# Performance work log

Measured on AMD Instinct MI355X. Metric: run time of the kernel, lower is better.

## Reference

```python
import jax, jax.numpy as jnp
import numpy as np

H = 2048          # hidden_size
M = 512           # moe_intermediate_size
E = 8             # n_routed_experts
TOP_K = 2         # num_experts_per_tok
N_SHARED = 2      # n_shared_experts -> shared intermediate = M * N_SHARED
MS = M * N_SHARED
B, S = 2, 1024


def setup_inputs() -> dict:
    key = jax.random.key(0)
    ks = jax.random.split(key, 9)
    sc = 0.02
    return {
        "hidden_states": jax.random.normal(ks[0], (B, S, H), dtype=jnp.float32),
        "gate_w": jax.random.normal(ks[1], (E, H), dtype=jnp.float32) * sc,
        "Wg": jax.random.normal(ks[2], (E, H, M), dtype=jnp.float32) * sc,   # gate_proj per expert
        "Wu": jax.random.normal(ks[3], (E, H, M), dtype=jnp.float32) * sc,   # up_proj per expert
        "Wd": jax.random.normal(ks[4], (E, M, H), dtype=jnp.float32) * sc,   # down_proj per expert
        "sWg": jax.random.normal(ks[5], (H, MS), dtype=jnp.float32) * sc,    # shared gate_proj
        "sWu": jax.random.normal(ks[6], (H, MS), dtype=jnp.float32) * sc,    # shared up_proj
        "sWd": jax.random.normal(ks[7], (MS, H), dtype=jnp.float32) * sc,    # shared down_proj
    }


def reference(hidden_states, gate_w, Wg, Wu, Wd, sWg, sWu, sWd):
    b, s, h = hidden_states.shape
    x = hidden_states.reshape(-1, h)                     # [N, H]
    n = x.shape[0]

    # --- MoEGate: top-k routing with softmax over the selected logits ---
    logits = x @ gate_w.T                                # [N, E]
    topk_vals, topk_idx = jax.lax.top_k(logits, TOP_K)   # [N, K]
    w = jax.nn.softmax(topk_vals, axis=-1)               # softmax scoring over top-k
    # per-token combine weight for every expert (zero where not routed)
    comb = jnp.zeros((n, E), x.dtype).at[jnp.arange(n)[:, None], topk_idx].add(w)

    # --- Routed experts (SwiGLU MLP per expert); combine is the sparse
    #     weight matrix `comb`, mathematically identical to torch dispatch ---
    g = jnp.einsum('nh,ehm->enm', x, Wg)                 # [E, N, M]
    u = jnp.einsum('nh,ehm->enm', x, Wu)
    eo = jnp.einsum('enm,emh->enh', jax.nn.silu(g) * u, Wd)  # [E, N, H]
    y = jnp.einsum('ne,enh->nh', comb, eo)               # weighted combine

    # --- Shared experts (dense SwiGLU MLP on all tokens) ---
    y = y + (jax.nn.silu(x @ sWg) * (x @ sWu)) @ sWd
    return y.reshape(b, s, h)
```

## Files before the change

kernel.cpp:

```cpp
#include <hip/hip_runtime.h>

#define H 2048
#define MDIM 512
#define NE 8
#define MS 1024
#define NTOK 2048
#define ACT_R_ROWS 5120

typedef unsigned short u16;
typedef __attribute__((ext_vector_type(8))) short s16x8;
typedef __attribute__((ext_vector_type(4))) float f32x4;

__device__ inline u16 f2bf(float f) {
  unsigned u = __builtin_bit_cast(unsigned, f);
  u = (u + 0x7fffu + ((u >> 16) & 1u)) >> 16;
  return (u16)u;
}
__device__ inline float bf2f(u16 v) {
  return __builtin_bit_cast(float, (unsigned)v << 16);
}

__device__ inline f32x4 mfma16(s16x8 a, s16x8 b, f32x4 c) {
  return __builtin_amdgcn_mfma_f32_16x16x32_bf16(a, b, c, 0, 0, 0);
}

__device__ inline void gload16(const void* g, void* l) {
  __builtin_amdgcn_global_load_lds(
      (const __attribute__((address_space(1))) unsigned int*)g,
      (__attribute__((address_space(3))) unsigned int*)l, 16, 0, 0);
}


__global__ void k_cvt(const float* __restrict__ src, u16* __restrict__ dst, int n8) {
  int i = blockIdx.x * 256 + threadIdx.x;
  if (i >= n8) return;
  const f32x4* s = (const f32x4*)src;
  f32x4 a = s[2 * i + 0], b = s[2 * i + 1];
  s16x8 o;
  o[0] = (short)f2bf(a[0]); o[1] = (short)f2bf(a[1]);
  o[2] = (short)f2bf(a[2]); o[3] = (short)f2bf(a[3]);
  o[4] = (short)f2bf(b[0]); o[5] = (short)f2bf(b[1]);
  o[6] = (short)f2bf(b[2]); o[7] = (short)f2bf(b[3]);
  ((s16x8*)dst)[i] = o;
}

__device__ inline void tile_t64(const float* __restrict__ src, u16* __restrict__ dst,
                                int R, int C, int bx, int by) {
  __shared__ u16 tt[64][66];
  int c0 = bx * 64, r0 = by * 64;
  int t = threadIdx.x;
  int cq = (t & 15) * 4, rr = t >> 4;
  #pragma unroll
  for (int i = 0; i < 4; i++) {
    int row = rr + i * 16;
    f32x4 v = *(const f32x4*)&src[(long)(r0 + row) * C + c0 + cq];
    tt[cq + 0][row] = f2bf(v[0]);
    tt[cq + 1][row] = f2bf(v[1]);
    tt[cq + 2][row] = f2bf(v[2]);
    tt[cq + 3][row] = f2bf(v[3]);
  }
  __syncthreads();
  int c = t >> 2, ch = t & 3;
  #pragma unroll
  for (int h = 0; h < 2; h++) {
    int chunk = ch + h * 4;
    const u16* p = &tt[c][chunk * 8];
    s16x8 o;
    #pragma unroll
    for (int w0 = 0; w0 < 8; w0++) o[w0] = (short)p[w0];
    *(s16x8*)&dst[(long)(c0 + c) * R + r0 + chunk * 8] = o;
  }
}

__global__ __launch_bounds__(256) void k_prep(
    const float* __restrict__ Wg, const float* __restrict__ Wu,
    const float* __restrict__ Wd, const float* __restrict__ sWg,
    const float* __restrict__ sWu, const float* __restrict__ sWd,
    u16* __restrict__ WgT, u16* __restrict__ WuT, u16* __restrict__ WdT,
    u16* __restrict__ sWgT, u16* __restrict__ sWuT, u16* __restrict__ sWdT) {
  int b = blockIdx.x;
  const float* src; u16* dst; int R, C, lb;
  if (b < 2048) {
    lb = b; R = H; C = MDIM;
    int z = lb >> 8; lb &= 255;
    src = Wg + (size_t)z * H * MDIM; dst = WgT + (size_t)z * MDIM * H;
  } else if (b < 4096) {
    lb = b - 2048; R = H; C = MDIM;
    int z = lb >> 8; lb &= 255;
    src = Wu + (size_t)z * H * MDIM; dst = WuT + (size_t)z * MDIM * H;
  } else if (b < 6144) {
    lb = b - 4096; R = MDIM; C = H;
    int z = lb >> 8; lb &= 255;
    src = Wd + (size_t)z * MDIM * H; dst = WdT + (size_t)z * H * MDIM;
  } else if (b < 6656) {
    lb = b - 6144; R = H; C = MS; src = sWg; dst = sWgT;
  } else if (b < 7168) {
    lb = b - 6656; R = H; C = MS; src = sWu; dst = sWuT;
  } else {
    lb = b - 7168; R = MS; C = H; src = sWd; dst = sWdT;
  }
  int nbx = C >> 6;
  tile_t64(src, dst, R, C, lb % nbx, lb / nbx);
}


__global__ void k_logits(const float* __restrict__ x, const float* __restrict__ gw,
                         int* __restrict__ te, float* __restrict__ tw) {
  int n = blockIdx.x * 4 + (threadIdx.x >> 6);
  int lane = threadIdx.x & 63;
  double acc[NE];
  #pragma unroll
  for (int e = 0; e < NE; e++) acc[e] = 0.0;
  for (int j = lane; j < H; j += 64) {
    float xv = x[(long)n * H + j];
    #pragma unroll
    for (int e = 0; e < NE; e++) acc[e] += (double)xv * (double)gw[e * H + j];
  }
  #pragma unroll
  for (int off = 32; off; off >>= 1) {
    #pragma unroll
    for (int e = 0; e < NE; e++) acc[e] += __shfl_xor(acc[e], off);
  }
  if (lane == 0) {
    int b0 = 0; double v0 = acc[0];
    #pragma unroll
    for (int e = 1; e < NE; e++) { if (acc[e] > v0) { v0 = acc[e]; b0 = e; } }
    int b1 = -1; double v1 = -1e300;
    #pragma unroll
    for (int e = 0; e < NE; e++) { if (e != b0 && acc[e] > v1) { v1 = acc[e]; b1 = e; } }
    double ex = exp(v1 - v0);
    te[n * 2] = b0; te[n * 2 + 1] = b1;
    tw[n * 2] = (float)(1.0 / (1.0 + ex));
    tw[n * 2 + 1] = (float)(ex / (1.0 + ex));
  }
}

__global__ __launch_bounds__(256) void k_build(
    const int* __restrict__ te, const float* __restrict__ tw,
    int* __restrict__ counts, int* __restrict__ offs,
    int* __restrict__ perm, float* __restrict__ wgt, int* __restrict__ slotmap) {
  __shared__ int cnt[256][NE];
  __shared__ int pb[NE];
  int t = threadIdx.x;
  int ebuf[16];
  int lc[NE];
  #pragma unroll
  for (int e = 0; e < NE; e++) lc[e] = 0;
  #pragma unroll
  for (int i = 0; i < 16; i++) {
    int ei = te[t * 16 + i];
    ebuf[i] = ei;
    #pragma unroll
    for (int e = 0; e < NE; e++) lc[e] += (ei == e) ? 1 : 0;
  }
  #pragma unroll
  for (int e = 0; e < NE; e++) cnt[t][e] = lc[e];
  __syncthreads();
  if (t < NE) {
    int run = 0;
    for (int i = 0; i < 256; i++) { int v = cnt[i][t]; cnt[i][t] = run; run += v; }
    counts[t] = run;
  }
  __syncthreads();
  if (t == 0) {
    int off = 0;
    #pragma unroll
    for (int e = 0; e < NE; e++) {
      pb[e] = off; offs[e] = off;
      off += ((counts[e] + 127) >> 7) << 7;
    }
    offs[NE] = off;
  }
  for (int i = t; i < ACT_R_ROWS; i += 256) { perm[i] = 0; wgt[i] = 0.f; }
  __syncthreads();
  int run2[NE];
  #pragma unroll
  for (int e = 0; e < NE; e++) run2[e] = cnt[t][e];
  #pragma unroll
  for (int i = 0; i < 16; i++) {
    int ei = ebuf[i];
    int idx = 0;
    #pragma unroll
    for (int e = 0; e < NE; e++) {
      if (ei == e) idx = pb[e] + run2[e];
      run2[e] += (ei == e) ? 1 : 0;
    }
    perm[idx] = (t * 16 + i) >> 1;
    wgt[idx] = tw[t * 16 + i];
    slotmap[t * 16 + i] = idx;
  }
}

__global__ __launch_bounds__(256, 2) void k_gu(
    const u16* __restrict__ xbf, const u16* __restrict__ WgT, const u16* __restrict__ WuT,
    const u16* __restrict__ sWgT, const u16* __restrict__ sWuT,
    u16* __restrict__ act_s, u16* __restrict__ act_r,
    const int* __restrict__ perm, const int* __restrict__ counts,
    const int* __restrict__ offs) {
  int lin = blockIdx.x;
  int xcd = lin & 7, jj = lin >> 3;
  int g = xcd + 8 * (jj % 10);
  int bx = jj / 10;
  const u16 *Bg, *Bu;
  u16* act;
  int Nout, cnt, rowBase, by;
  bool gather;
  if (g < 16) {
    gather = false; by = g;
    cnt = NTOK; rowBase = bx * 128;
    Bg = sWgT + (size_t)by * 64 * H;
    Bu = sWuT + (size_t)by * 64 * H;
    act = act_s; Nout = MS;
  } else {
    gather = true;
    int e = (g - 16) >> 3; by = (g - 16) & 7;
    cnt = counts[e];
    if (bx * 128 >= cnt) return;
    rowBase = offs[e] + bx * 128;
    Bg = WgT + ((size_t)e * MDIM + (size_t)by * 64) * H;
    Bu = WuT + ((size_t)e * MDIM + (size_t)by * 64) * H;
    act = act_r; Nout = MDIM;
  }

  __shared__ char lds[2][32768];

  int tid = threadIdx.x;
  int wave = tid >> 6, lane = tid & 63;
  int wr = wave >> 1, wc = wave & 1;
  int la = lane & 15, ks = lane >> 4;

  int rIn = tid >> 3;
  int csrc = ((tid & 7) << 4) ^ ((rIn & 7) << 4);
  const char* srcA[4];
  const char* srcBg[2];
  const char* srcBu[2];
  #pragma unroll
  for (int j = 0; j < 4; j++) {
    int row = j * 32 + rIn;
    int tok = gather ? perm[rowBase + row] : (rowBase + row);
    srcA[j] = (const char*)xbf + (size_t)tok * H * 2 + csrc;
  }
  #pragma unroll
  for (int j = 0; j < 2; j++) {
    int row = j * 32 + rIn;
    srcBg[j] = (const char*)Bg + (size_t)row * H * 2 + csrc;
    srcBu[j] = (const char*)Bu + (size_t)row * H * 2 + csrc;
  }

  int offA[4][2], offB[2][2];
  #pragma unroll
  for (int m = 0; m < 4; m++) {
    int arow = wr * 64 + m * 16 + la;
    #pragma unroll
    for (int kk = 0; kk < 2; kk++) {
      int c = kk * 64 + ks * 16;
      offA[m][kk] = arow * 128 + (c ^ ((arow & 7) << 4));
    }
  }
  #pragma unroll
  for (int n = 0; n < 2; n++) {
    int brow = wc * 32 + n * 16 + la;
    #pragma unroll
    for (int kk = 0; kk < 2; kk++) {
      int c = kk * 64 + ks * 16;
      offB[n][kk] = brow * 128 + (c ^ ((brow & 7) << 4));
    }
  }

  f32x4 zero4 = {0.f, 0.f, 0.f, 0.f};
  f32x4 gacc[4][2], uacc[4][2];
  #pragma unroll
  for (int m = 0; m < 4; m++)
    #pragma unroll
    for (int n = 0; n < 2; n++) { gacc[m][n] = zero4; uacc[m][n] = zero4; }

  auto STAGE = [&](int p, int k0) {
    char* b = lds[p];
    #pragma unroll
    for (int j = 0; j < 4; j++)
      gload16(srcA[j] + k0, b + j * 4096 + wave * 1024);
    #pragma unroll
    for (int j = 0; j < 2; j++) {
      gload16(srcBg[j] + k0, b + 16384 + j * 4096 + wave * 1024);
      gload16(srcBu[j] + k0, b + 24576 + j * 4096 + wave * 1024);
    }
  };

  const int NT = H / 64;
  STAGE(0, 0);
  STAGE(1, 128);
  asm volatile("s_waitcnt vmcnt(8)" ::: "memory");
  __builtin_amdgcn_sched_barrier(0);
  __builtin_amdgcn_s_barrier();

  for (int t = 0; t < NT; ++t) {
    int p = t & 1;
    const char* A = lds[p];
    const char* G = lds[p] + 16384;
    const char* U = lds[p] + 24576;
    s16x8 af[2][4], gf[2][2], uf[2][2];
    #pragma unroll
    for (int kk = 0; kk < 2; kk++) {
      #pragma unroll
      for (int m = 0; m < 4; m++) af[kk][m] = *(const s16x8*)(A + offA[m][kk]);
      #pragma unroll
      for (int n = 0; n < 2; n++) {
        gf[kk][n] = *(const s16x8*)(G + offB[n][kk]);
        uf[kk][n] = *(const s16x8*)(U + offB[n][kk]);
      }
    }
    asm volatile("s_waitcnt lgkmcnt(0)" ::: "memory");
    __builtin_amdgcn_sched_barrier(0);
    __builtin_amdgcn_s_barrier();
    if (t + 2 < NT) STAGE(p, (t + 2) * 128);
    __builtin_amdgcn_sched_barrier(0);
    #pragma unroll
    for (int kk = 0; kk < 2; kk++) {
      #pragma unroll
      for (int m = 0; m < 4; m++) {
        #pragma unroll
        for (int n = 0; n < 2; n++) {
          gacc[m][n] = mfma16(af[kk][m], gf[kk][n], gacc[m][n]);
          uacc[m][n] = mfma16(af[kk][m], uf[kk][n], uacc[m][n]);
        }
      }
    }
    if (t + 2 < NT) { asm volatile("s_waitcnt vmcnt(8)" ::: "memory"); }
    else            { asm volatile("s_waitcnt vmcnt(0)" ::: "memory"); }
    __builtin_amdgcn_sched_barrier(0);
    __builtin_amdgcn_s_barrier();
  }

  #pragma unroll
  for (int m = 0; m < 4; m++) {
    #pragma unroll
    for (int n = 0; n < 2; n++) {
      #pragma unroll
      for (int r = 0; r < 4; r++) {
        int lr = wr * 64 + m * 16 + ks * 4 + r;
        int col = by * 64 + wc * 32 + n * 16 + la;
        float gg = gacc[m][n][r], uu = uacc[m][n][r];
        float a = gg / (1.0f + __expf(-gg)) * uu;
        if (gather && (bx * 128 + lr) >= cnt) a = 0.0f;
        act[(size_t)(rowBase + lr) * Nout + col] = f2bf(a);
      }
    }
  }
}

__global__ __launch_bounds__(256, 3) void k_down2(
    const u16* __restrict__ act_s, const u16* __restrict__ act_r,
    const u16* __restrict__ sWdT, const u16* __restrict__ WdT,
    float* __restrict__ y, u16* __restrict__ rdown,
    const float* __restrict__ wgt,
    const int* __restrict__ counts, const int* __restrict__ offs) {
  int lin = blockIdx.x;
  int xcd = lin & 7, jj = lin >> 3;
  int g = xcd + 8 * (jj % 36);
  int bx = jj / 36;
  const u16 *A, *B;
  int KD, NT, cnt, rowBase, by;
  bool routed;
  if (g < 32) {
    routed = false; by = g;
    KD = MS; NT = MS / 64;
    cnt = NTOK; rowBase = bx * 128;
    A = act_s + (size_t)rowBase * MS;
    B = sWdT + (size_t)by * 64 * MS;
  } else {
    routed = true;
    int e = (g - 32) >> 5; by = (g - 32) & 31;
    KD = MDIM; NT = MDIM / 64;
    cnt = counts[e];
    if (bx * 128 >= cnt) return;
    rowBase = offs[e] + bx * 128;
    A = act_r + (size_t)rowBase * MDIM;
    B = WdT + ((size_t)e * H + (size_t)by * 64) * MDIM;
  }

  __shared__ char lds[2][24576];

  int tid = threadIdx.x;
  int wave = tid >> 6, lane = tid & 63;
  int wr = wave >> 1, wc = wave & 1;
  int la = lane & 15, ks = lane >> 4;

  int rIn = tid >> 3;
  int csrc = ((tid & 7) << 4) ^ ((rIn & 7) << 4);
  const char* srcA[4];
  const char* srcB[2];
  #pragma unroll
  for (int j = 0; j < 4; j++) {
    int row = j * 32 + rIn;
    srcA[j] = (const char*)A + (size_t)row * KD * 2 + csrc;
  }
  #pragma unroll
  for (int j = 0; j < 2; j++) {
    int row = j * 32 + rIn;
    srcB[j] = (const char*)B + (size_t)row * KD * 2 + csrc;
  }

  int offA[4][2], offB[2][2];
  #pragma unroll
  for (int m = 0; m < 4; m++) {
    int arow = wr * 64 + m * 16 + la;
    #pragma unroll
    for (int kk = 0; kk < 2; kk++) {
      int c = kk * 64 + ks * 16;
      offA[m][kk] = arow * 128 + (c ^ ((arow & 7) << 4));
    }
  }
  #pragma unroll
  for (int n = 0; n < 2; n++) {
    int brow = wc * 32 + n * 16 + la;
    #pragma unroll
    for (int kk = 0; kk < 2; kk++) {
      int c = kk * 64 + ks * 16;
      offB[n][kk] = brow * 128 + (c ^ ((brow & 7) << 4));
    }
  }

  f32x4 zero4 = {0.f, 0.f, 0.f, 0.f};
  f32x4 acc[4][2];
  #pragma unroll
  for (int m = 0; m < 4; m++)
    #pragma unroll
    for (int n = 0; n < 2; n++) acc[m][n] = zero4;

  auto STAGE = [&](int p, int k0) {
    char* b = lds[p];
    #pragma unroll
    for (int j = 0; j < 4; j++)
      gload16(srcA[j] + k0, b + j * 4096 + wave * 1024);
    #pragma unroll
    for (int j = 0; j < 2; j++)
      gload16(srcB[j] + k0, b + 16384 + j * 4096 + wave * 1024);
  };

  STAGE(0, 0);
  STAGE(1, 128);
  asm volatile("s_waitcnt vmcnt(6)" ::: "memory");
  __builtin_amdgcn_sched_barrier(0);
  __builtin_amdgcn_s_barrier();

  for (int t = 0; t < NT; ++t) {
    int p = t & 1;
    const char* Ab = lds[p];
    const char* Bb = lds[p] + 16384;
    s16x8 af[2][4], bf[2][2];
    #pragma unroll
    for (int kk = 0; kk < 2; kk++) {
      #pragma unroll
      for (int m = 0; m < 4; m++) af[kk][m] = *(const s16x8*)(Ab + offA[m][kk]);
      #pragma unroll
      for (int n = 0; n < 2; n++) bf[kk][n] = *(const s16x8*)(Bb + offB[n][kk]);
    }
    asm volatile("s_waitcnt lgkmcnt(0)" ::: "memory");
    __builtin_amdgcn_sched_barrier(0);
    __builtin_amdgcn_s_barrier();
    if (t + 2 < NT) STAGE(p, (t + 2) * 128);
    __builtin_amdgcn_sched_barrier(0);
    #pragma unroll
    for (int kk = 0; kk < 2; kk++) {
      #pragma unroll
      for (int m = 0; m < 4; m++)
        #pragma unroll
        for (int n = 0; n < 2; n++) acc[m][n] = mfma16(af[kk][m], bf[kk][n], acc[m][n]);
    }
    if (t + 2 < NT) { asm volatile("s_waitcnt vmcnt(6)" ::: "memory"); }
    else            { asm volatile("s_waitcnt vmcnt(0)" ::: "memory"); }
    __builtin_amdgcn_sched_barrier(0);
    __builtin_amdgcn_s_barrier();
  }

  #pragma unroll
  for (int m = 0; m < 4; m++) {
    #pragma unroll
    for (int n = 0; n < 2; n++) {
      #pragma unroll
      for (int r = 0; r < 4; r++) {
        int lr = wr * 64 + m * 16 + ks * 4 + r;
        int col = by * 64 + wc * 32 + n * 16 + la;
        float v = acc[m][n][r];
        if (routed) {
          if (bx * 128 + lr < cnt) {
            int si = rowBase + lr;
            rdown[(size_t)si * H + col] = f2bf(wgt[si] * v);
          }
        } else {
          y[(size_t)(rowBase + lr) * H + col] = v;
        }
      }
    }
  }
}

__global__ __launch_bounds__(256) void k_combine(float* __restrict__ y,
                                                 const u16* __restrict__ rdown,
                                                 const int* __restrict__ slotmap) {
  int n = blockIdx.x;
  int s0 = slotmap[n * 2], s1 = slotmap[n * 2 + 1];
  const s16x8* r0 = (const s16x8*)(rdown + (size_t)s0 * H);
  const s16x8* r1 = (const s16x8*)(rdown + (size_t)s1 * H);
  f32x4* yp = (f32x4*)(y + (size_t)n * H);
  int t = threadIdx.x;
  s16x8 a = r0[t], b = r1[t];
  f32x4 y0 = yp[2 * t], y1 = yp[2 * t + 1];
  #pragma unroll
  for (int j = 0; j < 4; j++) {
    y0[j] += bf2f((u16)a[j]) + bf2f((u16)b[j]);
    y1[j] += bf2f((u16)a[4 + j]) + bf2f((u16)b[4 + j]);
  }
  yp[2 * t] = y0;
  yp[2 * t + 1] = y1;
}


extern "C" void kernel_launch(void* const* d_in, const int* in_sizes, int n_in,
                              void* d_out, int out_size, void* d_ws, size_t ws_size,
                              hipStream_t stream) {
  const float* x   = (const float*)d_in[0];
  const float* gw  = (const float*)d_in[1];
  const float* Wg  = (const float*)d_in[2];
  const float* Wu  = (const float*)d_in[3];
  const float* Wd  = (const float*)d_in[4];
  const float* sWg = (const float*)d_in[5];
  const float* sWu = (const float*)d_in[6];
  const float* sWd = (const float*)d_in[7];
  float* y = (float*)d_out;

  char* w = (char*)d_ws;
  auto alloc = [&](size_t bytes) {
    char* p = w;
    w += (bytes + 255) & ~(size_t)255;
    return p;
  };
  u16* xbf   = (u16*)alloc((size_t)NTOK * H * 2);
  u16* WgT   = (u16*)alloc((size_t)NE * MDIM * H * 2);
  u16* WuT   = (u16*)alloc((size_t)NE * MDIM * H * 2);
  u16* WdT   = (u16*)alloc((size_t)NE * H * MDIM * 2);
  u16* sWgT  = (u16*)alloc((size_t)MS * H * 2);
  u16* sWuT  = (u16*)alloc((size_t)MS * H * 2);
  u16* sWdT  = (u16*)alloc((size_t)H * MS * 2);
  u16* act_s = (u16*)alloc((size_t)NTOK * MS * 2);
  u16* act_r = (u16*)alloc((size_t)ACT_R_ROWS * MDIM * 2);
  u16* rdown = (u16*)alloc((size_t)ACT_R_ROWS * H * 2);
  int*   te      = (int*)alloc((size_t)NTOK * 2 * 4);
  float* tw      = (float*)alloc((size_t)NTOK * 2 * 4);
  int*   counts  = (int*)alloc(64);
  int*   offs    = (int*)alloc(64);
  int*   perm    = (int*)alloc((size_t)ACT_R_ROWS * 4);
  float* wgt     = (float*)alloc((size_t)ACT_R_ROWS * 4);
  int*   slotmap = (int*)alloc((size_t)NTOK * 2 * 4);

  k_logits<<<NTOK / 4, 256, 0, stream>>>(x, gw, te, tw);
  k_build<<<1, 256, 0, stream>>>(te, tw, counts, offs, perm, wgt, slotmap);

  int n8 = NTOK * H / 8;
  k_cvt<<<(n8 + 255) / 256, 256, 0, stream>>>(x, xbf, n8);
  k_prep<<<7680, 256, 0, stream>>>(Wg, Wu, Wd, sWg, sWu, sWd,
                                   WgT, WuT, WdT, sWgT, sWuT, sWdT);

  k_gu<<<80 * 16, 256, 0, stream>>>(
      xbf, WgT, WuT, sWgT, sWuT, act_s, act_r, perm, counts, offs);

  k_down2<<<288 * 16, 256, 0, stream>>>(
      act_s, act_r, sWdT, WdT, y, rdown, wgt, counts, offs);

  k_combine<<<NTOK, 256, 0, stream>>>(y, rdown, slotmap);
}
```

Measured before the change: 168.6 us.

## Fuse x conversion into logits kernel; single-buffer GEMM LDS for higher occupancy

```diff
diff --git a/kernel.cpp b/kernel.cpp
--- a/kernel.cpp
+++ b/kernel.cpp
@@ -8,6 +8,7 @@
 #define ACT_R_ROWS 5120
 
 typedef unsigned short u16;
+typedef __attribute__((ext_vector_type(4))) short s16x4;
 typedef __attribute__((ext_vector_type(8))) short s16x8;
 typedef __attribute__((ext_vector_type(4))) float f32x4;
 
@@ -31,18 +32,107 @@
 }
 
 
-__global__ void k_cvt(const float* __restrict__ src, u16* __restrict__ dst, int n8) {
-  int i = blockIdx.x * 256 + threadIdx.x;
-  if (i >= n8) return;
-  const f32x4* s = (const f32x4*)src;
-  f32x4 a = s[2 * i + 0], b = s[2 * i + 1];
-  s16x8 o;
-  o[0] = (short)f2bf(a[0]); o[1] = (short)f2bf(a[1]);
-  o[2] = (short)f2bf(a[2]); o[3] = (short)f2bf(a[3]);
-  o[4] = (short)f2bf(b[0]); o[5] = (short)f2bf(b[1]);
-  o[6] = (short)f2bf(b[2]); o[7] = (short)f2bf(b[3]);
-  ((s16x8*)dst)[i] = o;
-}
+__global__ __launch_bounds__(256) void k_xlog(const float* __restrict__ x,
+                                              const float* __restrict__ gw,
+                                              u16* __restrict__ xbf,
+                                              int* __restrict__ te, float* __restrict__ tw) {
+  int n = blockIdx.x * 4 + (threadIdx.x >> 6);
+  int lane = threadIdx.x & 63;
+  double acc[NE];
+  #pragma unroll
+  for (int e = 0; e < NE; e++) acc[e] = 0.0;
+  const f32x4* xr = (const f32x4*)(x + (size_t)n * H);
+  s16x4* xo = (s16x4*)(xbf + (size_t)n * H);
+  #pragma unroll
+  for (int it = 0; it < H / 256; it++) {
+    int j4 = it * 64 + lane;
+    f32x4 v = xr[j4];
+    s16x4 o;
+    o[0] = (short)f2bf(v[0]); o[1] = (short)f2bf(v[1]);
+    o[2] = (short)f2bf(v[2]); o[3] = (short)f2bf(v[3]);
+    xo[j4] = o;
+    #pragma unroll
+    for (int e = 0; e < NE; e++) {
+      f32x4 g = *(const f32x4*)&gw[e * H + j4 * 4];
+      acc[e] += (double)v[0] * g[0] + (double)v[1] * g[1] +
+                (double)v[2] * g[2] + (double)v[3] * g[3];
+    }
+  }
+  #pragma unroll
+  for (int off = 32; off; off >>= 1) {
+    #pragma unroll
+    for (int e = 0; e < NE; e++) acc[e] += __shfl_xor(acc[e], off);
+  }
+  if (lane == 0) {
+    int b0 = 0; double v0 = acc[0];
+    #pragma unroll
+    for (int e = 1; e < NE; e++) { if (acc[e] > v0) { v0 = acc[e]; b0 = e; } }
+    int b1 = -1; double v1 = -1e300;
+    #pragma unroll
+    for (int e = 0; e < NE; e++) { if (e != b0 && acc[e] > v1) { v1 = acc[e]; b1 = e; } }
+    double ex = exp(v1 - v0);
+    te[n * 2] = b0; te[n * 2 + 1] = b1;
+    tw[n * 2] = (float)(1.0 / (1.0 + ex));
+    tw[n * 2 + 1] = (float)(ex / (1.0 + ex));
+  }
+}
+
+__global__ __launch_bounds__(256) void k_build(
+    const int* __restrict__ te, const float* __restrict__ tw,
+    int* __restrict__ counts, int* __restrict__ offs,
+    int* __restrict__ perm, float* __restrict__ wgt, int* __restrict__ slotmap) {
+  __shared__ int cnt[256][NE];
+  __shared__ int pb[NE];
+  int t = threadIdx.x;
+  int ebuf[16];
+  int lc[NE];
+  #pragma unroll
+  for (int e = 0; e < NE; e++) lc[e] = 0;
+  #pragma unroll
+  for (int i = 0; i < 16; i++) {
+    int ei = te[t * 16 + i];
+    ebuf[i] = ei;
+    #pragma unroll
+    for (int e = 0; e < NE; e++) lc[e] += (ei == e) ? 1 : 0;
+  }
+  #pragma unroll
+  for (int e = 0; e < NE; e++) cnt[t][e] = lc[e];
+  __syncthreads();
+  if (t < NE) {
+    int run = 0;
+    for (int i = 0; i < 256; i++) { int v = cnt[i][t]; cnt[i][t] = run; run += v; }
+    counts[t] = run;
+  }
+  __syncthreads();
+  if (t == 0) {
+    int off = 0;
+    #pragma unroll
+    for (int e = 0; e < NE; e++) {
+      pb[e] = off; offs[e] = off;
+      off += ((counts[e] + 127) >> 7) << 7;
+    }
+    offs[NE] = off;
+  }
+  for (int i = t; i < ACT_R_ROWS; i += 256) { perm[i] = 0; wgt[i] = 0.f; }
+  __syncthreads();
+  int run2[NE];
+  #pragma unroll
+  for (int e = 0; e < NE; e++) run2[e] = cnt[t][e];
+  #pragma unroll
+  for (int i = 0; i < 16; i++) {
+    int ei = ebuf[i];
+    int idx = 0;
+    #pragma unroll
+    for (int e = 0; e < NE; e++) {
+      if (ei == e) idx = pb[e] + run2[e];
+      run2[e] += (ei == e) ? 1 : 0;
+    }
+    perm[idx] = (t * 16 + i) >> 1;
+    wgt[idx] = tw[t * 16 + i];
+    slotmap[t * 16 + i] = idx;
+  }
+}
+
 
 __device__ inline void tile_t64(const float* __restrict__ src, u16* __restrict__ dst,
                                 int R, int C, int bx, int by) {
@@ -103,95 +193,7 @@
   tile_t64(src, dst, R, C, lb % nbx, lb / nbx);
 }
 
-
-__global__ void k_logits(const float* __restrict__ x, const float* __restrict__ gw,
-                         int* __restrict__ te, float* __restrict__ tw) {
-  int n = blockIdx.x * 4 + (threadIdx.x >> 6);
-  int lane = threadIdx.x & 63;
-  double acc[NE];
-  #pragma unroll
-  for (int e = 0; e < NE; e++) acc[e] = 0.0;
-  for (int j = lane; j < H; j += 64) {
-    float xv = x[(long)n * H + j];
-    #pragma unroll
-    for (int e = 0; e < NE; e++) acc[e] += (double)xv * (double)gw[e * H + j];
-  }
-  #pragma unroll
-  for (int off = 32; off; off >>= 1) {
-    #pragma unroll
-    for (int e = 0; e < NE; e++) acc[e] += __shfl_xor(acc[e], off);
-  }
-  if (lane == 0) {
-    int b0 = 0; double v0 = acc[0];
-    #pragma unroll
-    for (int e = 1; e < NE; e++) { if (acc[e] > v0) { v0 = acc[e]; b0 = e; } }
-    int b1 = -1; double v1 = -1e300;
-    #pragma unroll
-    for (int e = 0; e < NE; e++) { if (e != b0 && acc[e] > v1) { v1 = acc[e]; b1 = e; } }
-    double ex = exp(v1 - v0);
-    te[n * 2] = b0; te[n * 2 + 1] = b1;
-    tw[n * 2] = (float)(1.0 / (1.0 + ex));
-    tw[n * 2 + 1] = (float)(ex / (1.0 + ex));
-  }
-}
-
-__global__ __launch_bounds__(256) void k_build(
-    const int* __restrict__ te, const float* __restrict__ tw,
-    int* __restrict__ counts, int* __restrict__ offs,
-    int* __restrict__ perm, float* __restrict__ wgt, int* __restrict__ slotmap) {
-  __shared__ int cnt[256][NE];
-  __shared__ int pb[NE];
-  int t = threadIdx.x;
-  int ebuf[16];
-  int lc[NE];
-  #pragma unroll
-  for (int e = 0; e < NE; e++) lc[e] = 0;
-  #pragma unroll
-  for (int i = 0; i < 16; i++) {
-    int ei = te[t * 16 + i];
-    ebuf[i] = ei;
-    #pragma unroll
-    for (int e = 0; e < NE; e++) lc[e] += (ei == e) ? 1 : 0;
-  }
-  #pragma unroll
-  for (int e = 0; e < NE; e++) cnt[t][e] = lc[e];
-  __syncthreads();
-  if (t < NE) {
-    int run = 0;
-    for (int i = 0; i < 256; i++) { int v = cnt[i][t]; cnt[i][t] = run; run += v; }
-    counts[t] = run;
-  }
-  __syncthreads();
-  if (t == 0) {
-    int off = 0;
-    #pragma unroll
-    for (int e = 0; e < NE; e++) {
-      pb[e] = off; offs[e] = off;
-      off += ((counts[e] + 127) >> 7) << 7;
-    }
-    offs[NE] = off;
-  }
-  for (int i = t; i < ACT_R_ROWS; i += 256) { perm[i] = 0; wgt[i] = 0.f; }
-  __syncthreads();
-  int run2[NE];
-  #pragma unroll
-  for (int e = 0; e < NE; e++) run2[e] = cnt[t][e];
-  #pragma unroll
-  for (int i = 0; i < 16; i++) {
-    int ei = ebuf[i];
-    int idx = 0;
-    #pragma unroll
-    for (int e = 0; e < NE; e++) {
-      if (ei == e) idx = pb[e] + run2[e];
-      run2[e] += (ei == e) ? 1 : 0;
-    }
-    perm[idx] = (t * 16 + i) >> 1;
-    wgt[idx] = tw[t * 16 + i];
-    slotmap[t * 16 + i] = idx;
-  }
-}
-
-__global__ __launch_bounds__(256, 2) void k_gu(
+__global__ __launch_bounds__(256, 5) void k_gu(
     const u16* __restrict__ xbf, const u16* __restrict__ WgT, const u16* __restrict__ WuT,
     const u16* __restrict__ sWgT, const u16* __restrict__ sWuT,
     u16* __restrict__ act_s, u16* __restrict__ act_r,
@@ -222,7 +224,7 @@
     act = act_r; Nout = MDIM;
   }
 
-  __shared__ char lds[2][32768];
+  __shared__ char lds[32768];
 
   int tid = threadIdx.x;
   int wave = tid >> 6, lane = tid & 63;
@@ -274,59 +276,43 @@
     #pragma unroll
     for (int n = 0; n < 2; n++) { gacc[m][n] = zero4; uacc[m][n] = zero4; }
 
-  auto STAGE = [&](int p, int k0) {
-    char* b = lds[p];
+  auto STAGE = [&](int k0) {
     #pragma unroll
     for (int j = 0; j < 4; j++)
-      gload16(srcA[j] + k0, b + j * 4096 + wave * 1024);
+      gload16(srcA[j] + k0, lds + j * 4096 + wave * 1024);
     #pragma unroll
     for (int j = 0; j < 2; j++) {
-      gload16(srcBg[j] + k0, b + 16384 + j * 4096 + wave * 1024);
-      gload16(srcBu[j] + k0, b + 24576 + j * 4096 + wave * 1024);
+      gload16(srcBg[j] + k0, lds + 16384 + j * 4096 + wave * 1024);
+      gload16(srcBu[j] + k0, lds + 24576 + j * 4096 + wave * 1024);
     }
   };
 
   const int NT = H / 64;
-  STAGE(0, 0);
-  STAGE(1, 128);
-  asm volatile("s_waitcnt vmcnt(8)" ::: "memory");
-  __builtin_amdgcn_sched_barrier(0);
-  __builtin_amdgcn_s_barrier();
-
   for (int t = 0; t < NT; ++t) {
-    int p = t & 1;
-    const char* A = lds[p];
-    const char* G = lds[p] + 16384;
-    const char* U = lds[p] + 24576;
-    s16x8 af[2][4], gf[2][2], uf[2][2];
-    #pragma unroll
-    for (int kk = 0; kk < 2; kk++) {
-      #pragma unroll
-      for (int m = 0; m < 4; m++) af[kk][m] = *(const s16x8*)(A + offA[m][kk]);
-      #pragma unroll
-      for (int n = 0; n < 2; n++) {
-        gf[kk][n] = *(const s16x8*)(G + offB[n][kk]);
-        uf[kk][n] = *(const s16x8*)(U + offB[n][kk]);
-      }
-    }
-    asm volatile("s_waitcnt lgkmcnt(0)" ::: "memory");
+    STAGE(t * 128);
+    asm volatile("s_waitcnt vmcnt(0)" ::: "memory");
     __builtin_amdgcn_sched_barrier(0);
     __builtin_amdgcn_s_barrier();
-    if (t + 2 < NT) STAGE(p, (t + 2) * 128);
     __builtin_amdgcn_sched_barrier(0);
     #pragma unroll
     for (int kk = 0; kk < 2; kk++) {
+      s16x8 a[4], gf[2], uf[2];
+      #pragma unroll
+      for (int m = 0; m < 4; m++) a[m] = *(const s16x8*)(lds + offA[m][kk]);
+      #pragma unroll
+      for (int n = 0; n < 2; n++) {
+        gf[n] = *(const s16x8*)(lds + 16384 + offB[n][kk]);
+        uf[n] = *(const s16x8*)(lds + 24576 + offB[n][kk]);
+      }
       #pragma unroll
       for (int m = 0; m < 4; m++) {
         #pragma unroll
         for (int n = 0; n < 2; n++) {
-          gacc[m][n] = mfma16(af[kk][m], gf[kk][n], gacc[m][n]);
-          uacc[m][n] = mfma16(af[kk][m], uf[kk][n], uacc[m][n]);
+          gacc[m][n] = mfma16(a[m], gf[n], gacc[m][n]);
+          uacc[m][n] = mfma16(a[m], uf[n], uacc[m][n]);
         }
       }
     }
-    if (t + 2 < NT) { asm volatile("s_waitcnt vmcnt(8)" ::: "memory"); }
-    else            { asm volatile("s_waitcnt vmcnt(0)" ::: "memory"); }
     __builtin_amdgcn_sched_barrier(0);
     __builtin_amdgcn_s_barrier();
   }
@@ -348,7 +334,7 @@
   }
 }
 
-__global__ __launch_bounds__(256, 3) void k_down2(
+__global__ __launch_bounds__(256, 6) void k_down2(
     const u16* __restrict__ act_s, const u16* __restrict__ act_r,
     const u16* __restrict__ sWdT, const u16* __restrict__ WdT,
     float* __restrict__ y, u16* __restrict__ rdown,
@@ -378,7 +364,7 @@
     B = WdT + ((size_t)e * H + (size_t)by * 64) * MDIM;
   }
 
-  __shared__ char lds[2][24576];
+  __shared__ char lds[24576];
 
   int tid = threadIdx.x;
   int wave = tid >> 6, lane = tid & 63;
@@ -427,48 +413,33 @@
     #pragma unroll
     for (int n = 0; n < 2; n++) acc[m][n] = zero4;
 
-  auto STAGE = [&](int p, int k0) {
-    char* b = lds[p];
+  auto STAGE = [&](int k0) {
     #pragma unroll
     for (int j = 0; j < 4; j++)
-      gload16(srcA[j] + k0, b + j * 4096 + wave * 1024);
+      gload16(srcA[j] + k0, lds + j * 4096 + wave * 1024);
     #pragma unroll
     for (int j = 0; j < 2; j++)
-      gload16(srcB[j] + k0, b + 16384 + j * 4096 + wave * 1024);
+      gload16(srcB[j] + k0, lds + 16384 + j * 4096 + wave * 1024);
   };
 
-  STAGE(0, 0);
-  STAGE(1, 128);
-  asm volatile("s_waitcnt vmcnt(6)" ::: "memory");
-  __builtin_amdgcn_sched_barrier(0);
-  __builtin_amdgcn_s_barrier();
-
   for (int t = 0; t < NT; ++t) {
-    int p = t & 1;
-    const char* Ab = lds[p];
-    const char* Bb = lds[p] + 16384;
-    s16x8 af[2][4], bf[2][2];
-    #pragma unroll
-    for (int kk = 0; kk < 2; kk++) {
-      #pragma unroll
-      for (int m = 0; m < 4; m++) af[kk][m] = *(const s16x8*)(Ab + offA[m][kk]);
-      #pragma unroll
-      for (int n = 0; n < 2; n++) bf[kk][n] = *(const s16x8*)(Bb + offB[n][kk]);
-    }
-    asm volatile("s_waitcnt lgkmcnt(0)" ::: "memory");
+    STAGE(t * 128);
+    asm volatile("s_waitcnt vmcnt(0)" ::: "memory");
     __builtin_amdgcn_sched_barrier(0);
     __builtin_amdgcn_s_barrier();
-    if (t + 2 < NT) STAGE(p, (t + 2) * 128);
     __builtin_amdgcn_sched_barrier(0);
     #pragma unroll
     for (int kk = 0; kk < 2; kk++) {
+      s16x8 a[4], b[2];
+      #pragma unroll
+      for (int m = 0; m < 4; m++) a[m] = *(const s16x8*)(lds + offA[m][kk]);
+      #pragma unroll
+      for (int n = 0; n < 2; n++) b[n] = *(const s16x8*)(lds + 16384 + offB[n][kk]);
       #pragma unroll
       for (int m = 0; m < 4; m++)
         #pragma unroll
-        for (int n = 0; n < 2; n++) acc[m][n] = mfma16(af[kk][m], bf[kk][n], acc[m][n]);
-    }
-    if (t + 2 < NT) { asm volatile("s_waitcnt vmcnt(6)" ::: "memory"); }
-    else            { asm volatile("s_waitcnt vmcnt(0)" ::: "memory"); }
+        for (int n = 0; n < 2; n++) acc[m][n] = mfma16(a[m], b[n], acc[m][n]);
+    }
     __builtin_amdgcn_sched_barrier(0);
     __builtin_amdgcn_s_barrier();
   }
@@ -553,11 +524,9 @@
   float* wgt     = (float*)alloc((size_t)ACT_R_ROWS * 4);
   int*   slotmap = (int*)alloc((size_t)NTOK * 2 * 4);
 
-  k_logits<<<NTOK / 4, 256, 0, stream>>>(x, gw, te, tw);
+  k_xlog<<<NTOK / 4, 256, 0, stream>>>(x, gw, xbf, te, tw);
   k_build<<<1, 256, 0, stream>>>(te, tw, counts, offs, perm, wgt, slotmap);
 
-  int n8 = NTOK * H / 8;
-  k_cvt<<<(n8 + 255) / 256, 256, 0, stream>>>(x, xbf, n8);
   k_prep<<<7680, 256, 0, stream>>>(Wg, Wu, Wd, sWg, sWu, sWd,
                                    WgT, WuT, WdT, sWgT, sWuT, sWdT);
 
```

Measured after the change: 183.9 us. 9.1% more time.

## Fuse routing logits, x conversion and weight transposes into one front kernel

Applied to the files above, without the earlier changes.

```diff
diff --git a/kernel.cpp b/kernel.cpp
--- a/kernel.cpp
+++ b/kernel.cpp
@@ -8,6 +8,7 @@
 #define ACT_R_ROWS 5120
 
 typedef unsigned short u16;
+typedef __attribute__((ext_vector_type(4))) short s16x4;
 typedef __attribute__((ext_vector_type(8))) short s16x8;
 typedef __attribute__((ext_vector_type(4))) float f32x4;
 
@@ -31,22 +32,8 @@
 }
 
 
-__global__ void k_cvt(const float* __restrict__ src, u16* __restrict__ dst, int n8) {
-  int i = blockIdx.x * 256 + threadIdx.x;
-  if (i >= n8) return;
-  const f32x4* s = (const f32x4*)src;
-  f32x4 a = s[2 * i + 0], b = s[2 * i + 1];
-  s16x8 o;
-  o[0] = (short)f2bf(a[0]); o[1] = (short)f2bf(a[1]);
-  o[2] = (short)f2bf(a[2]); o[3] = (short)f2bf(a[3]);
-  o[4] = (short)f2bf(b[0]); o[5] = (short)f2bf(b[1]);
-  o[6] = (short)f2bf(b[2]); o[7] = (short)f2bf(b[3]);
-  ((s16x8*)dst)[i] = o;
-}
-
 __device__ inline void tile_t64(const float* __restrict__ src, u16* __restrict__ dst,
-                                int R, int C, int bx, int by) {
-  __shared__ u16 tt[64][66];
+                                int R, int C, int bx, int by, u16 (*tt)[66]) {
   int c0 = bx * 64, r0 = by * 64;
   int t = threadIdx.x;
   int cq = (t & 15) * 4, rr = t >> 4;
@@ -72,13 +59,59 @@
   }
 }
 
-__global__ __launch_bounds__(256) void k_prep(
+__global__ __launch_bounds__(256) void k_front(
+    const float* __restrict__ x, const float* __restrict__ gw,
+    u16* __restrict__ xbf, int* __restrict__ te, float* __restrict__ tw,
     const float* __restrict__ Wg, const float* __restrict__ Wu,
     const float* __restrict__ Wd, const float* __restrict__ sWg,
     const float* __restrict__ sWu, const float* __restrict__ sWd,
     u16* __restrict__ WgT, u16* __restrict__ WuT, u16* __restrict__ WdT,
     u16* __restrict__ sWgT, u16* __restrict__ sWuT, u16* __restrict__ sWdT) {
-  int b = blockIdx.x;
+  __shared__ u16 tt[64][66];
+  int blk = blockIdx.x;
+  if (blk < NTOK / 4) {
+    int n = blk * 4 + (threadIdx.x >> 6);
+    int lane = threadIdx.x & 63;
+    double acc[NE];
+    #pragma unroll
+    for (int e = 0; e < NE; e++) acc[e] = 0.0;
+    const f32x4* xr = (const f32x4*)(x + (size_t)n * H);
+    s16x4* xo = (s16x4*)(xbf + (size_t)n * H);
+    #pragma unroll
+    for (int it = 0; it < H / 256; it++) {
+      int j4 = it * 64 + lane;
+      f32x4 v = xr[j4];
+      s16x4 o;
+      o[0] = (short)f2bf(v[0]); o[1] = (short)f2bf(v[1]);
+      o[2] = (short)f2bf(v[2]); o[3] = (short)f2bf(v[3]);
+      xo[j4] = o;
+      #pragma unroll
+      for (int e = 0; e < NE; e++) {
+        f32x4 g = *(const f32x4*)&gw[e * H + j4 * 4];
+        acc[e] += (double)v[0] * g[0] + (double)v[1] * g[1] +
+                  (double)v[2] * g[2] + (double)v[3] * g[3];
+      }
+    }
+    #pragma unroll
+    for (int off = 32; off; off >>= 1) {
+      #pragma unroll
+      for (int e = 0; e < NE; e++) acc[e] += __shfl_xor(acc[e], off);
+    }
+    if (lane == 0) {
+      int b0 = 0; double v0 = acc[0];
+      #pragma unroll
+      for (int e = 1; e < NE; e++) { if (acc[e] > v0) { v0 = acc[e]; b0 = e; } }
+      int b1 = -1; double v1 = -1e300;
+      #pragma unroll
+      for (int e = 0; e < NE; e++) { if (e != b0 && acc[e] > v1) { v1 = acc[e]; b1 = e; } }
+      double ex = exp(v1 - v0);
+      te[n * 2] = b0; te[n * 2 + 1] = b1;
+      tw[n * 2] = (float)(1.0 / (1.0 + ex));
+      tw[n * 2 + 1] = (float)(ex / (1.0 + ex));
+    }
+    return;
+  }
+  int b = blk - NTOK / 4;
   const float* src; u16* dst; int R, C, lb;
   if (b < 2048) {
     lb = b; R = H; C = MDIM;
@@ -100,39 +133,7 @@
     lb = b - 7168; R = MS; C = H; src = sWd; dst = sWdT;
   }
   int nbx = C >> 6;
-  tile_t64(src, dst, R, C, lb % nbx, lb / nbx);
-}
-
-
-__global__ void k_logits(const float* __restrict__ x, const float* __restrict__ gw,
-                         int* __restrict__ te, float* __restrict__ tw) {
-  int n = blockIdx.x * 4 + (threadIdx.x >> 6);
-  int lane = threadIdx.x & 63;
-  double acc[NE];
-  #pragma unroll
-  for (int e = 0; e < NE; e++) acc[e] = 0.0;
-  for (int j = lane; j < H; j += 64) {
-    float xv = x[(long)n * H + j];
-    #pragma unroll
-    for (int e = 0; e < NE; e++) acc[e] += (double)xv * (double)gw[e * H + j];
-  }
-  #pragma unroll
-  for (int off = 32; off; off >>= 1) {
-    #pragma unroll
-    for (int e = 0; e < NE; e++) acc[e] += __shfl_xor(acc[e], off);
-  }
-  if (lane == 0) {
-    int b0 = 0; double v0 = acc[0];
-    #pragma unroll
-    for (int e = 1; e < NE; e++) { if (acc[e] > v0) { v0 = acc[e]; b0 = e; } }
-    int b1 = -1; double v1 = -1e300;
-    #pragma unroll
-    for (int e = 0; e < NE; e++) { if (e != b0 && acc[e] > v1) { v1 = acc[e]; b1 = e; } }
-    double ex = exp(v1 - v0);
-    te[n * 2] = b0; te[n * 2 + 1] = b1;
-    tw[n * 2] = (float)(1.0 / (1.0 + ex));
-    tw[n * 2 + 1] = (float)(ex / (1.0 + ex));
-  }
+  tile_t64(src, dst, R, C, lb % nbx, lb / nbx, tt);
 }
 
 __global__ __launch_bounds__(256) void k_build(
@@ -314,6 +315,7 @@
     __builtin_amdgcn_s_barrier();
     if (t + 2 < NT) STAGE(p, (t + 2) * 128);
     __builtin_amdgcn_sched_barrier(0);
+    __builtin_amdgcn_s_setprio(1);
     #pragma unroll
     for (int kk = 0; kk < 2; kk++) {
       #pragma unroll
@@ -325,6 +327,7 @@
         }
       }
     }
+    __builtin_amdgcn_s_setprio(0);
     if (t + 2 < NT) { asm volatile("s_waitcnt vmcnt(8)" ::: "memory"); }
     else            { asm volatile("s_waitcnt vmcnt(0)" ::: "memory"); }
     __builtin_amdgcn_sched_barrier(0);
@@ -460,6 +463,7 @@
     __builtin_amdgcn_s_barrier();
     if (t + 2 < NT) STAGE(p, (t + 2) * 128);
     __builtin_amdgcn_sched_barrier(0);
+    __builtin_amdgcn_s_setprio(1);
     #pragma unroll
     for (int kk = 0; kk < 2; kk++) {
       #pragma unroll
@@ -467,6 +471,7 @@
         #pragma unroll
         for (int n = 0; n < 2; n++) acc[m][n] = mfma16(af[kk][m], bf[kk][n], acc[m][n]);
     }
+    __builtin_amdgcn_s_setprio(0);
     if (t + 2 < NT) { asm volatile("s_waitcnt vmcnt(6)" ::: "memory"); }
     else            { asm volatile("s_waitcnt vmcnt(0)" ::: "memory"); }
     __builtin_amdgcn_sched_barrier(0);
@@ -553,13 +558,11 @@
   float* wgt     = (float*)alloc((size_t)ACT_R_ROWS * 4);
   int*   slotmap = (int*)alloc((size_t)NTOK * 2 * 4);
 
-  k_logits<<<NTOK / 4, 256, 0, stream>>>(x, gw, te, tw);
+  k_front<<<NTOK / 4 + 7680, 256, 0, stream>>>(
+      x, gw, xbf, te, tw, Wg, Wu, Wd, sWg, sWu, sWd,
+      WgT, WuT, WdT, sWgT, sWuT, sWdT);
+
   k_build<<<1, 256, 0, stream>>>(te, tw, counts, offs, perm, wgt, slotmap);
-
-  int n8 = NTOK * H / 8;
-  k_cvt<<<(n8 + 255) / 256, 256, 0, stream>>>(x, xbf, n8);
-  k_prep<<<7680, 256, 0, stream>>>(Wg, Wu, Wd, sWg, sWu, sWd,
-                                   WgT, WuT, WdT, sWgT, sWuT, sWdT);
 
   k_gu<<<80 * 16, 256, 0, stream>>>(
       xbf, WgT, WuT, sWgT, sWuT, act_s, act_r, perm, counts, offs);
```

New measurement: 149.0 us. 11.7% less time.
